# Kernel optimization log

Measured on AMD Instinct MI355X. Metric: run time of the kernel, lower is better.

The kernel has to match this reference:

```python
import jax, jax.numpy as jnp
import numpy as np

N = 8192
F_IN = 256
F_OUT = 64
ALPHA = 0.2  # LeakyReLU negative slope
NEG_INF = -9e15


def setup_inputs() -> dict:
    key = jax.random.key(0)
    k1, k2, k3, k4 = jax.random.split(key, 4)
    h = jax.random.normal(k1, (N, F_IN), dtype=jnp.float32)
    adj = jax.random.randint(k2, (N, N), 0, 2, dtype=jnp.int32)
    W = jax.random.normal(k3, (F_IN, F_OUT), dtype=jnp.float32) * 0.1
    a = jax.random.normal(k4, (2 * F_OUT, 1), dtype=jnp.float32) * 0.1
    return {"h": h, "adj": adj, "W": W, "a": a}


def reference(h, adj, W, a):
    # Wh: [N, F_out]
    Wh = h @ W
    # e_ij = LeakyReLU(a1 . Wh_i + a2 . Wh_j); same math as the O(N^2*2F)
    # concat in the original, computed via two [N] gathers + broadcast add.
    f_src = Wh @ a[:F_OUT, 0]   # [N] contribution of node i (row)
    f_dst = Wh @ a[F_OUT:, 0]   # [N] contribution of node j (col)
    e = f_src[:, None] + f_dst[None, :]          # [N, N]
    e = jnp.where(e > 0, e, ALPHA * e)           # LeakyReLU
    # masked softmax over neighbors (dim=1)
    e = jnp.where(adj > 0, e, NEG_INF)
    attention = jax.nn.softmax(e, axis=1)        # [N, N]
    h_prime = attention @ Wh                     # [N, F_out]
    # concat=True -> ELU
    return jax.nn.elu(h_prime)
```

## Files before the change

kernel.cpp:

```cpp
#include <hip/hip_runtime.h>
#include <math.h>

#define N 8192
#define FIN 256
#define FOUT 64
#define ALPHA 0.2f
#define LOG2E 1.442695040888963f

#define FMPITCH 65
#define FMWORDS (64 * FMPITCH)
#define SMEM_BYTES 33280

typedef float f32x4 __attribute__((ext_vector_type(4)));
typedef _Float16 f16x8 __attribute__((ext_vector_type(8)));

union F16V { uint4 u; f16x8 h; };

__device__ __forceinline__ unsigned pack_f16(float a, float b) {
    union { _Float16 h; unsigned short u; } ca, cb;
    ca.h = (_Float16)a; cb.h = (_Float16)b;
    return (unsigned)ca.u | ((unsigned)cb.u << 16);
}
__device__ __forceinline__ float wcalc(unsigned av, float fsr, float g) {
    float e = fsr + g;
    float le = e > 0.f ? e : ALPHA * e;
    float r = __builtin_exp2f(fmaf(le, LOG2E, -4.0f));
    return av != 0u ? r : 0.f;
}

__global__ __launch_bounds__(512) void gat_prep(
    const float* __restrict__ h, const float* __restrict__ W,
    const float* __restrict__ a,
    float* __restrict__ fsrc, float* __restrict__ fdst,
    uint4* __restrict__ Bp)
{
    __shared__ float sWh[32][FOUT + 1];
    const int t = threadIdx.x;
    const int f = t & 63;
    const int wq = t >> 6;
    const int row0 = blockIdx.x * 32;
    const int rbase = row0 + wq * 4;

    float acc[4] = {0.f, 0.f, 0.f, 0.f};
    for (int k0 = 0; k0 < FIN; k0 += 4) {
        const float w0 = W[(k0 + 0) * FOUT + f];
        const float w1 = W[(k0 + 1) * FOUT + f];
        const float w2 = W[(k0 + 2) * FOUT + f];
        const float w3 = W[(k0 + 3) * FOUT + f];
#pragma unroll
        for (int rr = 0; rr < 4; ++rr) {
            const float4 hv = *reinterpret_cast<const float4*>(
                &h[(size_t)(rbase + rr) * FIN + k0]);
            acc[rr] = fmaf(hv.x, w0, acc[rr]);
            acc[rr] = fmaf(hv.y, w1, acc[rr]);
            acc[rr] = fmaf(hv.z, w2, acc[rr]);
            acc[rr] = fmaf(hv.w, w3, acc[rr]);
        }
    }
    const float as = a[f], ad = a[FOUT + f];
#pragma unroll
    for (int rr = 0; rr < 4; ++rr) {
        sWh[wq * 4 + rr][f] = acc[rr];
        float fs = acc[rr] * as, fd = acc[rr] * ad;
#pragma unroll
        for (int off = 1; off < 64; off <<= 1) {
            fs += __shfl_xor(fs, off, 64);
            fd += __shfl_xor(fd, off, 64);
        }
        if (f == 0) { fsrc[rbase + rr] = fs; fdst[rbase + rr] = fd; }
    }
    __syncthreads();
    if (t < 256) {
        const int ft = t >> 6;
        const int l = t & 63;
        const int li = l & 15, g = l >> 4;
        float v[8];
#pragma unroll
        for (int e = 0; e < 8; ++e) v[e] = sWh[g * 8 + e][ft * 16 + li];
        uint4 pk;
        pk.x = pack_f16(v[0], v[1]);
        pk.y = pack_f16(v[2], v[3]);
        pk.z = pack_f16(v[4], v[5]);
        pk.w = pack_f16(v[6], v[7]);
        Bp[(size_t)(blockIdx.x * 4 + ft) * 64 + l] = pk;
    }
}

struct Regs { float4 g0, g1; uint4 b0, b1, b2, b3; };

__global__ __launch_bounds__(512, 4) void gat_main(
    const int* __restrict__ adj,
    const uint4* __restrict__ Bp,
    const float* __restrict__ fsrc, const float* __restrict__ fdst,
    float* __restrict__ out)
{
    __shared__ __align__(16) char smem[SMEM_BYTES];

    const int t = threadIdx.x;
    const int l = t & 63;
    const int w = t >> 6;
    const int row0 = blockIdx.x * 16;
    unsigned* fm = reinterpret_cast<unsigned*>(smem);

    {
        const int srow = t >> 5;
        const int c5 = t & 31;
        const int c0 = c5 >> 2;
        const int slot = c5 & 3;
        const int lcons = slot * 16 + srow;
        const size_t adjrow = (size_t)(row0 + srow) * N;
#pragma unroll
        for (int w8 = 0; w8 < 8; ++w8) {
            unsigned a32 = 0;
#pragma unroll
            for (int q = 0; q < 4; ++q) {
                const size_t o = adjrow + (w8 * 4 + q) * 256 + c5 * 8;
                const int4 v0 = *reinterpret_cast<const int4*>(&adj[o]);
                const int4 v1 = *reinterpret_cast<const int4*>(&adj[o + 4]);
                unsigned m = 0;
                m |= (v0.x != 0) ? 1u : 0u;
                m |= (v0.y != 0) ? 2u : 0u;
                m |= (v0.z != 0) ? 4u : 0u;
                m |= (v0.w != 0) ? 8u : 0u;
                m |= (v1.x != 0) ? 16u : 0u;
                m |= (v1.y != 0) ? 32u : 0u;
                m |= (v1.z != 0) ? 64u : 0u;
                m |= (v1.w != 0) ? 128u : 0u;
                a32 |= m << (8 * q);
            }
            fm[(w8 * 8 + c0) * FMPITCH + lcons] = a32;
        }
    }

    const int r = l & 15;
    const int kg8 = (l >> 4) << 3;
    const int jwbase = w * 1024;
    const int cgbase = w * 32;
    const float fsr = fsrc[row0 + r];

    f32x4 acc0 = {0.f, 0.f, 0.f, 0.f};
    f32x4 acc1 = {0.f, 0.f, 0.f, 0.f};
    f32x4 acc2 = {0.f, 0.f, 0.f, 0.f};
    f32x4 acc3 = {0.f, 0.f, 0.f, 0.f};
    float zacc = 0.f;
    Regs RA, RB;

#define CL(c) (((c) & 3) * 8 + ((c) >> 2))

#define LOADG(c, S)                                                            \
    {                                                                          \
        const int cl_ = CL(c);                                                 \
        const int j0_ = jwbase + cl_ * 32;                                     \
        S.g0 = *reinterpret_cast<const float4*>(&fdst[j0_ + kg8]);             \
        S.g1 = *reinterpret_cast<const float4*>(&fdst[j0_ + kg8 + 4]);         \
        const uint4* bp_ = Bp + (size_t)(cgbase + cl_) * 4 * 64 + l;           \
        S.b0 = bp_[0];                                                         \
        S.b1 = bp_[64];                                                        \
        S.b2 = bp_[128];                                                       \
        S.b3 = bp_[192];                                                       \
    }

#define COMPUTE(c, S)                                                          \
    {                                                                          \
        const unsigned m8 = (fmw[(c) >> 2] >> (8 * ((c) & 3))) & 0xffu;        \
        const float w0 = wcalc(m8 & 1u,   fsr, S.g0.x);                        \
        const float w1 = wcalc(m8 & 2u,   fsr, S.g0.y);                        \
        const float w2 = wcalc(m8 & 4u,   fsr, S.g0.z);                        \
        const float w3 = wcalc(m8 & 8u,   fsr, S.g0.w);                        \
        const float w4 = wcalc(m8 & 16u,  fsr, S.g1.x);                        \
        const float w5 = wcalc(m8 & 32u,  fsr, S.g1.y);                        \
        const float w6 = wcalc(m8 & 64u,  fsr, S.g1.z);                        \
        const float w7 = wcalc(m8 & 128u, fsr, S.g1.w);                        \
        zacc += (w0 + w1) + (w2 + w3) + ((w4 + w5) + (w6 + w7));               \
        F16V av, b0v, b1v, b2v, b3v;                                           \
        av.u.x = pack_f16(w0, w1); av.u.y = pack_f16(w2, w3);                  \
        av.u.z = pack_f16(w4, w5); av.u.w = pack_f16(w6, w7);                  \
        b0v.u = S.b0; b1v.u = S.b1; b2v.u = S.b2; b3v.u = S.b3;                \
        __builtin_amdgcn_s_setprio(1);                                         \
        acc0 = __builtin_amdgcn_mfma_f32_16x16x32_f16(av.h, b0v.h, acc0, 0, 0, 0); \
        acc1 = __builtin_amdgcn_mfma_f32_16x16x32_f16(av.h, b1v.h, acc1, 0, 0, 0); \
        acc2 = __builtin_amdgcn_mfma_f32_16x16x32_f16(av.h, b2v.h, acc2, 0, 0, 0); \
        acc3 = __builtin_amdgcn_mfma_f32_16x16x32_f16(av.h, b3v.h, acc3, 0, 0, 0); \
        __builtin_amdgcn_s_setprio(0);                                         \
    }

    LOADG(0, RA);
    LOADG(1, RB);
    asm volatile("s_waitcnt lgkmcnt(0)" ::: "memory");
    __builtin_amdgcn_s_barrier();

    unsigned fmw[8];
#pragma unroll
    for (int g = 0; g < 8; ++g) fmw[g] = fm[(w * 8 + g) * FMPITCH + l];

#pragma unroll
    for (int c = 0; c < 32; c += 2) {
        COMPUTE(c, RA);
        if (c + 2 < 32) LOADG(c + 2, RA);
        COMPUTE(c + 1, RB);
        if (c + 3 < 32) LOADG(c + 3, RB);
    }
#undef LOADG
#undef COMPUTE
#undef CL

    float* accbuf = reinterpret_cast<float*>(smem);
    float* zbuf = reinterpret_cast<float*>(smem + 32768);
    __shared__ float Zfin[16];

    zacc += __shfl_xor(zacc, 16, 64);
    zacc += __shfl_xor(zacc, 32, 64);
    __syncthreads();
    if (l < 16) zbuf[w * 16 + l] = zacc;
    *reinterpret_cast<f32x4*>(&accbuf[((w * 4 + 0) * 64 + l) * 4]) = acc0;
    *reinterpret_cast<f32x4*>(&accbuf[((w * 4 + 1) * 64 + l) * 4]) = acc1;
    *reinterpret_cast<f32x4*>(&accbuf[((w * 4 + 2) * 64 + l) * 4]) = acc2;
    *reinterpret_cast<f32x4*>(&accbuf[((w * 4 + 3) * 64 + l) * 4]) = acc3;
    __syncthreads();
    if (t < 16) {
        float z = 0.f;
#pragma unroll
        for (int w2 = 0; w2 < 8; ++w2) z += zbuf[w2 * 16 + t];
        Zfin[t] = z;
    }
    __syncthreads();

#pragma unroll
    for (int e0 = 0; e0 < 2; ++e0) {
        const int e = t + e0 * 512;
        const int rr = e >> 6, f2 = e & 63;
        const int c = f2 >> 4;
        const int ln = (f2 & 15) | ((rr >> 2) << 4);
        const int rg = rr & 3;
        float s = 0.f;
#pragma unroll
        for (int w2 = 0; w2 < 8; ++w2)
            s += accbuf[((w2 * 4 + c) * 64 + ln) * 4 + rg];
        const float hp = s / Zfin[rr];
        out[(size_t)(row0 + rr) * FOUT + f2] = hp > 0.f ? hp : expm1f(hp);
    }
}

extern "C" void kernel_launch(void* const* d_in, const int* in_sizes, int n_in,
                              void* d_out, int out_size, void* d_ws, size_t ws_size,
                              hipStream_t stream) {
    const float* h   = (const float*)d_in[0];
    const int*   adj = (const int*)d_in[1];
    const float* W   = (const float*)d_in[2];
    const float* a   = (const float*)d_in[3];
    float* out = (float*)d_out;

    float* ws = (float*)d_ws;
    float* fsrc = ws;
    float* fdst = fsrc + N;
    uint4* Bp = (uint4*)(fdst + N);

    gat_prep<<<dim3(N / 32), dim3(512), 0, stream>>>(h, W, a, fsrc, fdst, Bp);
    gat_main<<<dim3(N / 16), dim3(512), 0, stream>>>(adj, Bp, fsrc, fdst, out);
}
```

Measured before the change: 103.5 us.

## Move adjacency bitmask packing into prep kernel and stream mask words per chunk

The prep kernel gains 16384 extra blocks that read the int32 adjacency matrix and pack it into an 8-bit-per-8-neighbours mask in workspace. The main kernel then reads this compact mask (16 rows x 1024 bytes) instead of the full int32 adjacency rows, stages it in shared memory with a new pitch, and reads one mask word per chunk inside the pipelined loop. The chunk ordering changes from an interleaved mapping to a linear one. The full adjacency read still happens once, but now in a separate pass with an extra mask write and read, trading the in-kernel packing cost for an extra global round trip.

```diff
diff --git a/kernel.cpp b/kernel.cpp
--- a/kernel.cpp
+++ b/kernel.cpp
@@ -7,8 +7,7 @@
 #define ALPHA 0.2f
 #define LOG2E 1.442695040888963f
 
-#define FMPITCH 65
-#define FMWORDS (64 * FMPITCH)
+#define MPITCH 260
 #define SMEM_BYTES 33280
 
 typedef float f32x4 __attribute__((ext_vector_type(4)));
@@ -30,12 +29,30 @@
 
 __global__ __launch_bounds__(512) void gat_prep(
     const float* __restrict__ h, const float* __restrict__ W,
-    const float* __restrict__ a,
+    const float* __restrict__ a, const int* __restrict__ adj,
     float* __restrict__ fsrc, float* __restrict__ fdst,
-    uint4* __restrict__ Bp)
+    uint4* __restrict__ Bp, unsigned char* __restrict__ mask8)
 {
     __shared__ float sWh[32][FOUT + 1];
     const int t = threadIdx.x;
+
+    if (blockIdx.x >= 256) {
+        const size_t tid = (size_t)(blockIdx.x - 256) * 512 + t;
+        const int4 v0 = *reinterpret_cast<const int4*>(&adj[tid * 8]);
+        const int4 v1 = *reinterpret_cast<const int4*>(&adj[tid * 8 + 4]);
+        unsigned m = 0;
+        m |= (v0.x != 0) ? 1u : 0u;
+        m |= (v0.y != 0) ? 2u : 0u;
+        m |= (v0.z != 0) ? 4u : 0u;
+        m |= (v0.w != 0) ? 8u : 0u;
+        m |= (v1.x != 0) ? 16u : 0u;
+        m |= (v1.y != 0) ? 32u : 0u;
+        m |= (v1.z != 0) ? 64u : 0u;
+        m |= (v1.w != 0) ? 128u : 0u;
+        mask8[tid] = (unsigned char)m;
+        return;
+    }
+
     const int f = t & 63;
     const int wq = t >> 6;
     const int row0 = blockIdx.x * 32;
@@ -86,57 +103,33 @@
     }
 }
 
-struct Regs { float4 g0, g1; uint4 b0, b1, b2, b3; };
+struct Regs { unsigned mw; float4 g0, g1; uint4 b0, b1, b2, b3; };
 
 __global__ __launch_bounds__(512, 4) void gat_main(
-    const int* __restrict__ adj,
+    const unsigned char* __restrict__ mask8,
     const uint4* __restrict__ Bp,
     const float* __restrict__ fsrc, const float* __restrict__ fdst,
     float* __restrict__ out)
 {
     __shared__ __align__(16) char smem[SMEM_BYTES];
+    unsigned* M32 = reinterpret_cast<unsigned*>(smem);
 
     const int t = threadIdx.x;
     const int l = t & 63;
     const int w = t >> 6;
     const int row0 = blockIdx.x * 16;
-    unsigned* fm = reinterpret_cast<unsigned*>(smem);
-
-    {
-        const int srow = t >> 5;
-        const int c5 = t & 31;
-        const int c0 = c5 >> 2;
-        const int slot = c5 & 3;
-        const int lcons = slot * 16 + srow;
-        const size_t adjrow = (size_t)(row0 + srow) * N;
-#pragma unroll
-        for (int w8 = 0; w8 < 8; ++w8) {
-            unsigned a32 = 0;
-#pragma unroll
-            for (int q = 0; q < 4; ++q) {
-                const size_t o = adjrow + (w8 * 4 + q) * 256 + c5 * 8;
-                const int4 v0 = *reinterpret_cast<const int4*>(&adj[o]);
-                const int4 v1 = *reinterpret_cast<const int4*>(&adj[o + 4]);
-                unsigned m = 0;
-                m |= (v0.x != 0) ? 1u : 0u;
-                m |= (v0.y != 0) ? 2u : 0u;
-                m |= (v0.z != 0) ? 4u : 0u;
-                m |= (v0.w != 0) ? 8u : 0u;
-                m |= (v1.x != 0) ? 16u : 0u;
-                m |= (v1.y != 0) ? 32u : 0u;
-                m |= (v1.z != 0) ? 64u : 0u;
-                m |= (v1.w != 0) ? 128u : 0u;
-                a32 |= m << (8 * q);
-            }
-            fm[(w8 * 8 + c0) * FMPITCH + lcons] = a32;
-        }
-    }
 
     const int r = l & 15;
-    const int kg8 = (l >> 4) << 3;
+    const int g16 = l >> 4;
+    const int kg8 = g16 << 3;
     const int jwbase = w * 1024;
     const int cgbase = w * 32;
     const float fsr = fsrc[row0 + r];
+    const int mbase = r * MPITCH + w * 32;
+    const int shft = g16 * 8;
+
+    const uint4 s0 = *reinterpret_cast<const uint4*>(&mask8[(size_t)row0 * 1024 + t * 32]);
+    const uint4 s1 = *reinterpret_cast<const uint4*>(&mask8[(size_t)row0 * 1024 + t * 32 + 16]);
 
     f32x4 acc0 = {0.f, 0.f, 0.f, 0.f};
     f32x4 acc1 = {0.f, 0.f, 0.f, 0.f};
@@ -145,24 +138,23 @@
     float zacc = 0.f;
     Regs RA, RB;
 
-#define CL(c) (((c) & 3) * 8 + ((c) >> 2))
-
 #define LOADG(c, S)                                                            \
     {                                                                          \
-        const int cl_ = CL(c);                                                 \
-        const int j0_ = jwbase + cl_ * 32;                                     \
+        const int j0_ = jwbase + (c) * 32;                                     \
         S.g0 = *reinterpret_cast<const float4*>(&fdst[j0_ + kg8]);             \
         S.g1 = *reinterpret_cast<const float4*>(&fdst[j0_ + kg8 + 4]);         \
-        const uint4* bp_ = Bp + (size_t)(cgbase + cl_) * 4 * 64 + l;           \
+        const uint4* bp_ = Bp + (size_t)(cgbase + (c)) * 4 * 64 + l;           \
         S.b0 = bp_[0];                                                         \
         S.b1 = bp_[64];                                                        \
         S.b2 = bp_[128];                                                       \
         S.b3 = bp_[192];                                                       \
     }
 
-#define COMPUTE(c, S)                                                          \
+#define MREAD(c, S) { S.mw = M32[mbase + (c)]; }
+
+#define COMPUTE(S)                                                             \
     {                                                                          \
-        const unsigned m8 = (fmw[(c) >> 2] >> (8 * ((c) & 3))) & 0xffu;        \
+        const unsigned m8 = (S.mw >> shft) & 0xffu;                            \
         const float w0 = wcalc(m8 & 1u,   fsr, S.g0.x);                        \
         const float w1 = wcalc(m8 & 2u,   fsr, S.g0.y);                        \
         const float w2 = wcalc(m8 & 4u,   fsr, S.g0.z);                        \
@@ -186,23 +178,29 @@
 
     LOADG(0, RA);
     LOADG(1, RB);
+
+    {
+        const int mrow = t >> 5;
+        const int w0i = (t & 31) * 8;
+        char* dst = smem + (mrow * MPITCH + w0i) * 4;
+        *reinterpret_cast<uint4*>(dst) = s0;
+        *reinterpret_cast<uint4*>(dst + 16) = s1;
+    }
     asm volatile("s_waitcnt lgkmcnt(0)" ::: "memory");
     __builtin_amdgcn_s_barrier();
 
-    unsigned fmw[8];
-#pragma unroll
-    for (int g = 0; g < 8; ++g) fmw[g] = fm[(w * 8 + g) * FMPITCH + l];
-
+    MREAD(0, RA);
+    MREAD(1, RB);
 #pragma unroll
     for (int c = 0; c < 32; c += 2) {
-        COMPUTE(c, RA);
-        if (c + 2 < 32) LOADG(c + 2, RA);
-        COMPUTE(c + 1, RB);
-        if (c + 3 < 32) LOADG(c + 3, RB);
+        COMPUTE(RA);
+        if (c + 2 < 32) { LOADG(c + 2, RA); MREAD(c + 2, RA); }
+        COMPUTE(RB);
+        if (c + 3 < 32) { LOADG(c + 3, RB); MREAD(c + 3, RB); }
     }
 #undef LOADG
+#undef MREAD
 #undef COMPUTE
-#undef CL
 
     float* accbuf = reinterpret_cast<float*>(smem);
     float* zbuf = reinterpret_cast<float*>(smem + 32768);
@@ -254,7 +252,10 @@
     float* fsrc = ws;
     float* fdst = fsrc + N;
     uint4* Bp = (uint4*)(fdst + N);
-
-    gat_prep<<<dim3(N / 32), dim3(512), 0, stream>>>(h, W, a, fsrc, fdst, Bp);
-    gat_main<<<dim3(N / 16), dim3(512), 0, stream>>>(adj, Bp, fsrc, fdst, out);
-}
+    unsigned char* mask8 = (unsigned char*)(Bp + 65536);
+
+    gat_prep<<<dim3(256 + 16384), dim3(512), 0, stream>>>(
+        h, W, a, adj, fsrc, fdst, Bp, mask8);
+    gat_main<<<dim3(N / 16), dim3(512), 0, stream>>>(
+        mask8, Bp, fsrc, fdst, out);
+}
```

Result: faster. 98.52 us (-4.8%).
